# Kernel optimization log

Hardware: AMD Instinct MI355X
Metric: run time of the kernel (lower is better)

The kernel has to match this reference:

```python
import jax, jax.numpy as jnp
import numpy as np

B, T, D, H, E = 2, 1024, 1024, 4096, 8


def setup_inputs() -> dict:
    key = jax.random.key(0)
    ks = jax.random.split(key, 6)
    x = jax.random.normal(ks[0], (B, T, D), dtype=jnp.float32)
    padding_mask = jnp.zeros((B, T), dtype=bool)
    # Gate: Linear(D, E, bias=False) -> weight (E, D)
    Wg = jax.random.normal(ks[1], (E, D), dtype=jnp.float32) * (1.0 / np.sqrt(D))
    # Stacked expert FFN params (torch Linear layout: weight (out, in))
    W1 = jax.random.normal(ks[2], (E, H, D), dtype=jnp.float32) * (1.0 / np.sqrt(D))
    b1 = jax.random.normal(ks[3], (E, H), dtype=jnp.float32) * 0.01
    W2 = jax.random.normal(ks[4], (E, D, H), dtype=jnp.float32) * (1.0 / np.sqrt(H))
    b2 = jax.random.normal(ks[5], (E, D), dtype=jnp.float32) * 0.01
    return {"x": x, "padding_mask": padding_mask, "Wg": Wg, "W1": W1, "b1": b1, "W2": W2, "b2": b2}


def _top2_gate(xt, pm, Wg):
    # xt: (nt, D) flattened tokens, pm: (nt,) bool padding mask
    nt, ec = xt.shape[0], Wg.shape[0]
    logits = (xt @ Wg.T).astype(jnp.float32)            # use_fp32=True
    gate_value = jax.nn.softmax(logits, axis=-1)        # (nt, E)
    gate_value = jnp.where(pm[:, None], 0.0, gate_value)
    top2_idx = jax.lax.top_k(gate_value, 2)[1]          # (nt, 2)
    keep = jax.nn.one_hot(top2_idx, ec, dtype=bool).any(axis=1)  # (nt, E) True at top1/top2
    gate_weights = jnp.where(keep, gate_value, 0.0)
    s = gate_weights.sum(axis=1, keepdims=True)
    s = jnp.where(s == 0.0, 1.0, s)
    gate_weights = gate_weights / s
    # load-balance loss: fraction of top-1 assignments vs mean gate prob per expert
    nt_real = (~pm).sum().astype(jnp.float32)
    top1_counts = (jax.nn.one_hot(top2_idx[:, 0], ec, dtype=jnp.float32)
                   * (~pm)[:, None].astype(jnp.float32)).sum(axis=0)  # (E,)
    lb_loss = ec * ((top1_counts / nt_real) * (gate_value.sum(axis=0) / nt_real)).sum()
    return lb_loss, gate_weights, gate_value


def reference(x, padding_mask, Wg, W1, b1, W2, b2):
    Bx, Tx, Dx = x.shape
    xt = x.reshape(-1, Dx)                   # (nt, D)
    pm = padding_mask.reshape(-1)            # (nt,)
    lb_loss, gw, gate_value = _top2_gate(xt, pm, Wg)
    gw = gw.astype(x.dtype)                  # (nt, E)
    # Expert FFNs (dense over experts; routing weights are zero except top-2)
    h = jax.nn.relu(jnp.einsum('nd,ehd->neh', xt, W1) + b1)   # (nt, E, H)
    y = jnp.einsum('neh,edh->ned', h, W2) + b2                # (nt, E, D)
    out = jnp.einsum('ne,ned->nd', gw, y).reshape(Bx, Tx, Dx)
    return out, gate_value, lb_loss
```

## Files before the change

kernel.cpp:

```cpp
#include <hip/hip_runtime.h>
#include <hip/hip_bf16.h>
#include <stdint.h>


#define NTOK 2048
#define DDIM 1024
#define HDIM 4096
#define NEXP 8
#define KSPLIT 2
#define CONVB 1024
#define GATEB (NTOK / 4)
#define ZEROB 512

typedef float  f32x4  __attribute__((ext_vector_type(4)));
typedef __bf16 bf16x8 __attribute__((ext_vector_type(8)));
typedef __bf16 bf16x4 __attribute__((ext_vector_type(4)));

typedef const __attribute__((address_space(1))) void g1_t;
typedef __attribute__((address_space(3))) void l3_t;
__device__ __forceinline__ void gld16(const void* g, void* l) {
  __builtin_amdgcn_global_load_lds((g1_t*)g, (l3_t*)l, 16, 0, 0);
}

__device__ __forceinline__ void conv_body(int bid, const float* __restrict__ src,
                                          __bf16* __restrict__ dst, long n8) {
  long i = (long)bid * 256 + threadIdx.x;
  long stride = (long)CONVB * 256;
  for (; i < n8; i += stride) {
    f32x4 a = ((const f32x4*)src)[2 * i];
    f32x4 b = ((const f32x4*)src)[2 * i + 1];
    bf16x8 o;
#pragma unroll
    for (int q = 0; q < 4; ++q) { o[q] = (__bf16)a[q]; o[q + 4] = (__bf16)b[q]; }
    ((bf16x8*)dst)[i] = o;
  }
}

__device__ __forceinline__ void zero_body(int bid, float* __restrict__ y, long n4) {
  long i = (long)bid * 256 + threadIdx.x;
  long stride = (long)ZEROB * 256;
  for (; i < n4; i += stride) ((f32x4*)y)[i] = (f32x4){0.f, 0.f, 0.f, 0.f};
}

__device__ __forceinline__ void gate_body(int bid, const float* __restrict__ x,
                                          const unsigned char* __restrict__ pmask,
                                          const float* __restrict__ Wg,
                                          float* __restrict__ gate_out,
                                          int* __restrict__ tix, float* __restrict__ twt,
                                          __bf16* __restrict__ xbf) {
  int wave = threadIdx.x >> 6, lane = threadIdx.x & 63;
  int t = bid * 4 + wave;
  const f32x4* x4 = (const f32x4*)(x + (size_t)t * DDIM);
  const f32x4* w4 = (const f32x4*)Wg;
  bf16x4* xb4 = (bf16x4*)(xbf + (size_t)t * DDIM);
  float acc[NEXP];
#pragma unroll
  for (int e = 0; e < NEXP; ++e) acc[e] = 0.f;
#pragma unroll
  for (int i = 0; i < 4; ++i) {
    f32x4 xv = x4[i * 64 + lane];
    bf16x4 xo;
#pragma unroll
    for (int q = 0; q < 4; ++q) xo[q] = (__bf16)xv[q];
    xb4[i * 64 + lane] = xo;
#pragma unroll
    for (int e = 0; e < NEXP; ++e) {
      f32x4 wv = w4[e * 256 + i * 64 + lane];
      acc[e] += xv[0]*wv[0] + xv[1]*wv[1] + xv[2]*wv[2] + xv[3]*wv[3];
    }
  }
#pragma unroll
  for (int e = 0; e < NEXP; ++e) {
    float v = acc[e];
#pragma unroll
    for (int off = 32; off > 0; off >>= 1) v += __shfl_xor(v, off, 64);
    acc[e] = v;
  }
  if (lane == 0) {
    bool pm = pmask[t] != 0;
    float m = acc[0];
#pragma unroll
    for (int e = 1; e < NEXP; ++e) m = fmaxf(m, acc[e]);
    float g[NEXP]; float s = 0.f;
#pragma unroll
    for (int e = 0; e < NEXP; ++e) { g[e] = expf(acc[e] - m); s += g[e]; }
    float inv = 1.f / s;
#pragma unroll
    for (int e = 0; e < NEXP; ++e) g[e] *= inv;
    if (pm) {
#pragma unroll
      for (int e = 0; e < NEXP; ++e) g[e] = 0.f;
    }
    int i1 = 0;
#pragma unroll
    for (int e = 1; e < NEXP; ++e) if (g[e] > g[i1]) i1 = e;
    int i2 = -1;
#pragma unroll
    for (int e = 0; e < NEXP; ++e) if (e != i1 && (i2 < 0 || g[e] > g[i2])) i2 = e;
    float w1 = g[i1], w2 = g[i2], ss = w1 + w2;
    if (ss == 0.f) ss = 1.f;
    w1 /= ss; w2 /= ss;
#pragma unroll
    for (int e = 0; e < NEXP; ++e) gate_out[(size_t)t * NEXP + e] = g[e];
    tix[2*t] = i1; tix[2*t+1] = i2;
    twt[2*t] = w1; twt[2*t+1] = w2;
  }
}

__global__ __launch_bounds__(256)
void preA_kernel(const float* __restrict__ x, const unsigned char* __restrict__ pmask,
                 const float* __restrict__ Wg, float* __restrict__ gate_out,
                 int* __restrict__ tix, float* __restrict__ twt,
                 __bf16* __restrict__ xbf, const float* __restrict__ W1,
                 __bf16* __restrict__ w1bf, float* __restrict__ out)
{
  int bid = blockIdx.x;
  if (bid < CONVB) { conv_body(bid, W1, w1bf, (long)NEXP * HDIM * DDIM / 8); return; }
  bid -= CONVB;
  if (bid < GATEB) { gate_body(bid, x, pmask, Wg, gate_out, tix, twt, xbf); return; }
  bid -= GATEB;
  zero_body(bid, out, (long)NTOK * DDIM / 4);
}

__global__ __launch_bounds__(256)
void conv_kernel(const float* __restrict__ src, __bf16* __restrict__ dst, long n8)
{
  conv_body(blockIdx.x, src, dst, n8);
}

__global__ __launch_bounds__(1024)
void stats_kernel(const float* __restrict__ gate_out, const int* __restrict__ tix,
                  const unsigned char* __restrict__ pmask,
                  int* __restrict__ ecount, int* __restrict__ offs,
                  int* __restrict__ fill, float* __restrict__ lb_out)
{
  int tid = threadIdx.x, lane = tid & 63, wv = tid >> 6;
  float lg[NEXP]; float lt1[NEXP]; int lec[NEXP]; float ln = 0.f;
#pragma unroll
  for (int e = 0; e < NEXP; ++e) { lg[e] = 0.f; lt1[e] = 0.f; lec[e] = 0; }
#pragma unroll
  for (int it = 0; it < NTOK / 1024; ++it) {
    int t = tid + it * 1024;
    f32x4 g0 = ((const f32x4*)(gate_out + (size_t)t * NEXP))[0];
    f32x4 g1 = ((const f32x4*)(gate_out + (size_t)t * NEXP))[1];
    lg[0] += g0[0]; lg[1] += g0[1]; lg[2] += g0[2]; lg[3] += g0[3];
    lg[4] += g1[0]; lg[5] += g1[1]; lg[6] += g1[2]; lg[7] += g1[3];
    if (!pmask[t]) {
      int i1 = tix[2*t], i2 = tix[2*t+1];
      lt1[i1] += 1.f; lec[i1] += 1; lec[i2] += 1; ln += 1.f;
    }
  }
#pragma unroll
  for (int e = 0; e < NEXP; ++e) {
#pragma unroll
    for (int off = 32; off > 0; off >>= 1) {
      lg[e]  += __shfl_xor(lg[e],  off, 64);
      lt1[e] += __shfl_xor(lt1[e], off, 64);
      lec[e] += __shfl_xor(lec[e], off, 64);
    }
  }
#pragma unroll
  for (int off = 32; off > 0; off >>= 1) ln += __shfl_xor(ln, off, 64);
  __shared__ float sg[16][NEXP], st[16][NEXP], sn[16];
  __shared__ int   se[16][NEXP];
  if (lane == 0) {
#pragma unroll
    for (int e = 0; e < NEXP; ++e) { sg[wv][e] = lg[e]; st[wv][e] = lt1[e]; se[wv][e] = lec[e]; }
    sn[wv] = ln;
  }
  __syncthreads();
  if (tid == 0) {
    float G[NEXP] = {0}, T1[NEXP] = {0}; int EC[NEXP] = {0}; float N = 0.f;
    for (int w = 0; w < 16; ++w) {
      N += sn[w];
#pragma unroll
      for (int e = 0; e < NEXP; ++e) { G[e] += sg[w][e]; T1[e] += st[w][e]; EC[e] += se[w][e]; }
    }
    int o = 0;
    for (int e = 0; e < NEXP; ++e) { ecount[e] = EC[e]; offs[e] = o; o += EC[e]; fill[e] = 0; }
    if (N <= 0.f) N = 1.f;
    float lb = 0.f;
    for (int e = 0; e < NEXP; ++e) lb += (T1[e] / N) * (G[e] / N);
    lb_out[0] = (float)NEXP * lb;
  }
}

__global__ __launch_bounds__(256)
void compact_kernel(const unsigned char* __restrict__ pmask, const int* __restrict__ tix,
                    const float* __restrict__ twt, const int* __restrict__ offs,
                    int* __restrict__ fill, int* __restrict__ tok_list,
                    float* __restrict__ wgt_list)
{
  int t = blockIdx.x * 256 + threadIdx.x;
  int lane = threadIdx.x & 63;
  bool pm = pmask[t] != 0;
#pragma unroll
  for (int j = 0; j < 2; ++j) {
    int e = pm ? -1 : tix[2*t + j];
    int pos = -1;
#pragma unroll
    for (int ex = 0; ex < NEXP; ++ex) {
      unsigned long long mask = __ballot(e == ex);
      if (mask) {
        int leader = (int)(__ffsll((long long)mask) - 1);
        int base = 0;
        if (lane == leader) base = atomicAdd(&fill[ex], (int)__popcll(mask));
        base = __shfl(base, leader, 64);
        if (e == ex)
          pos = offs[ex] + base + (int)__popcll(mask & ((1ull << lane) - 1ull));
      }
    }
    if (e >= 0) { tok_list[pos] = t; wgt_list[pos] = twt[2*t + j]; }
  }
}


__global__ __launch_bounds__(256)
void gemm1_kernel(const __bf16* __restrict__ xbf, const __bf16* __restrict__ w1bf,
                  const float* __restrict__ b1, const int* __restrict__ ecount,
                  const int* __restrict__ offs, const int* __restrict__ tok_list,
                  __bf16* __restrict__ hbuf)
{
  const int NTILE = HDIM / 128;
  const int MTILE = NTOK / 128;
  int bid = blockIdx.x;
  int e = bid / (MTILE * NTILE);
  int rem = bid % (MTILE * NTILE);
  int mt = rem / NTILE, nt = rem % NTILE;
  int cnt = ecount[e];
  if (mt * 128 >= cnt) return;
  int off = offs[e];

  __shared__ __bf16 As[3][128 * 32];
  __shared__ __bf16 Bs[3][128 * 32];

  int tid = threadIdx.x, lane = tid & 63, wave = tid >> 6;
  int wm = wave >> 1, wn = wave & 1;

  const __bf16* aP[2];
  const __bf16* bP[2];
#pragma unroll
  for (int c = 0; c < 2; ++c) {
    int row = c * 64 + (tid >> 2);
    int cd = (tid & 3) ^ ((row >> 1) & 3);
    int mrow = mt * 128 + row;
    int tok = tok_list[off + ((mrow < cnt) ? mrow : 0)];
    aP[c] = xbf + (size_t)tok * DDIM + cd * 8;
    bP[c] = w1bf + (size_t)e * HDIM * DDIM + (size_t)(nt * 128 + row) * DDIM + cd * 8;
  }
  int cg = ((lane >> 4) ^ ((lane >> 1) & 3)) << 3;

  f32x4 acc[4][4];
#pragma unroll
  for (int m = 0; m < 4; ++m)
#pragma unroll
    for (int n = 0; n < 4; ++n) acc[m][n] = (f32x4){0.f, 0.f, 0.f, 0.f};

  const int NIT = DDIM / 32;
#pragma unroll
  for (int pt = 0; pt < 2; ++pt)
#pragma unroll
    for (int c = 0; c < 2; ++c) {
      gld16(aP[c] + pt * 32, &As[pt][(c * 64 + wave * 16) * 32]);
      gld16(bP[c] + pt * 32, &Bs[pt][(c * 64 + wave * 16) * 32]);
    }

  for (int it = 0; it < NIT; ++it) {
    int cur = it % 3;
    if (it + 1 < NIT) asm volatile("s_waitcnt vmcnt(4)" ::: "memory");
    else              asm volatile("s_waitcnt vmcnt(0)" ::: "memory");
    __builtin_amdgcn_s_barrier();
    __builtin_amdgcn_sched_barrier(0);
    if (it + 2 < NIT) {
      int nb = (it + 2) % 3;
      int k0 = (it + 2) * 32;
#pragma unroll
      for (int c = 0; c < 2; ++c) {
        gld16(aP[c] + k0, &As[nb][(c * 64 + wave * 16) * 32]);
        gld16(bP[c] + k0, &Bs[nb][(c * 64 + wave * 16) * 32]);
      }
    }
    bf16x8 af[4], bfr[4];
#pragma unroll
    for (int m = 0; m < 4; ++m) af[m]  = *(const bf16x8*)&As[cur][(wm*64 + m*16 + (lane & 15)) * 32 + cg];
#pragma unroll
    for (int n = 0; n < 4; ++n) bfr[n] = *(const bf16x8*)&Bs[cur][(wn*64 + n*16 + (lane & 15)) * 32 + cg];
#pragma unroll
    for (int m = 0; m < 4; ++m)
#pragma unroll
      for (int n = 0; n < 4; ++n)
        acc[m][n] = __builtin_amdgcn_mfma_f32_16x16x32_bf16(af[m], bfr[n], acc[m][n], 0, 0, 0);
  }

#pragma unroll
  for (int n = 0; n < 4; ++n) {
    int col = nt * 128 + wn * 64 + n * 16 + (lane & 15);
    float bias = b1[e * HDIM + col];
#pragma unroll
    for (int m = 0; m < 4; ++m) {
#pragma unroll
      for (int j = 0; j < 4; ++j) {
        int mr = mt * 128 + wm * 64 + m * 16 + ((lane >> 4) << 2) + j;
        if (mr < cnt) {
          float v = fmaxf(acc[m][n][j] + bias, 0.f);
          hbuf[(size_t)(off + mr) * HDIM + col] = (__bf16)v;
        }
      }
    }
  }
}

__global__ __launch_bounds__(256)
void gemm2_kernel(const __bf16* __restrict__ hbuf, const __bf16* __restrict__ w2bf,
                  const float* __restrict__ b2, const int* __restrict__ ecount,
                  const int* __restrict__ offs, const int* __restrict__ tok_list,
                  const float* __restrict__ wgt_list, float* __restrict__ out)
{
  const int NTILE = DDIM / 128;
  const int MTILE = NTOK / 128;
  int bid = blockIdx.x;
  int e = bid / (MTILE * NTILE * KSPLIT);
  int rem = bid % (MTILE * NTILE * KSPLIT);
  int mt = rem / (NTILE * KSPLIT);
  int rem2 = rem % (NTILE * KSPLIT);
  int nt = rem2 / KSPLIT, kc = rem2 % KSPLIT;
  int cnt = ecount[e];
  if (mt * 128 >= cnt) return;
  int off = offs[e];

  __shared__ __bf16 As[3][128 * 32];
  __shared__ __bf16 Bs[3][128 * 32];

  int tid = threadIdx.x, lane = tid & 63, wave = tid >> 6;
  int wm = wave >> 1, wn = wave & 1;

  const __bf16* aP[2];
  const __bf16* bP[2];
#pragma unroll
  for (int c = 0; c < 2; ++c) {
    int row = c * 64 + (tid >> 2);
    int cd = (tid & 3) ^ ((row >> 1) & 3);
    aP[c] = hbuf + (size_t)(off + mt * 128 + row) * HDIM + cd * 8;
    bP[c] = w2bf + (size_t)e * DDIM * HDIM + (size_t)(nt * 128 + row) * HDIM + cd * 8;
  }
  int cg = ((lane >> 4) ^ ((lane >> 1) & 3)) << 3;

  f32x4 acc[4][4];
#pragma unroll
  for (int m = 0; m < 4; ++m)
#pragma unroll
    for (int n = 0; n < 4; ++n) acc[m][n] = (f32x4){0.f, 0.f, 0.f, 0.f};

  const int KCH = HDIM / KSPLIT;
  const int NIT = KCH / 32;
  int kbeg = kc * KCH;
#pragma unroll
  for (int pt = 0; pt < 2; ++pt)
#pragma unroll
    for (int c = 0; c < 2; ++c) {
      gld16(aP[c] + kbeg + pt * 32, &As[pt][(c * 64 + wave * 16) * 32]);
      gld16(bP[c] + kbeg + pt * 32, &Bs[pt][(c * 64 + wave * 16) * 32]);
    }

  for (int it = 0; it < NIT; ++it) {
    int cur = it % 3;
    if (it + 1 < NIT) asm volatile("s_waitcnt vmcnt(4)" ::: "memory");
    else              asm volatile("s_waitcnt vmcnt(0)" ::: "memory");
    __builtin_amdgcn_s_barrier();
    __builtin_amdgcn_sched_barrier(0);
    if (it + 2 < NIT) {
      int nb = (it + 2) % 3;
      int k0 = kbeg + (it + 2) * 32;
#pragma unroll
      for (int c = 0; c < 2; ++c) {
        gld16(aP[c] + k0, &As[nb][(c * 64 + wave * 16) * 32]);
        gld16(bP[c] + k0, &Bs[nb][(c * 64 + wave * 16) * 32]);
      }
    }
    bf16x8 af[4], bfr[4];
#pragma unroll
    for (int m = 0; m < 4; ++m) af[m]  = *(const bf16x8*)&As[cur][(wm*64 + m*16 + (lane & 15)) * 32 + cg];
#pragma unroll
    for (int n = 0; n < 4; ++n) bfr[n] = *(const bf16x8*)&Bs[cur][(wn*64 + n*16 + (lane & 15)) * 32 + cg];
#pragma unroll
    for (int m = 0; m < 4; ++m)
#pragma unroll
      for (int n = 0; n < 4; ++n)
        acc[m][n] = __builtin_amdgcn_mfma_f32_16x16x32_bf16(af[m], bfr[n], acc[m][n], 0, 0, 0);
  }

  float b2v[4];
#pragma unroll
  for (int n = 0; n < 4; ++n) {
    int col = nt * 128 + wn * 64 + n * 16 + (lane & 15);
    b2v[n] = (kc == 0) ? b2[e * DDIM + col] : 0.f;
  }
#pragma unroll
  for (int m = 0; m < 4; ++m) {
#pragma unroll
    for (int j = 0; j < 4; ++j) {
      int mr = mt * 128 + wm * 64 + m * 16 + ((lane >> 4) << 2) + j;
      if (mr >= cnt) continue;
      int slot = off + mr;
      int tok = tok_list[slot];
      float w = wgt_list[slot];
      float* obase = out + (size_t)tok * DDIM;
#pragma unroll
      for (int n = 0; n < 4; ++n) {
        int col = nt * 128 + wn * 64 + n * 16 + (lane & 15);
        atomicAdd(obase + col, w * (acc[m][n][j] + b2v[n]));
      }
    }
  }
}

extern "C" void kernel_launch(void* const* d_in, const int* in_sizes, int n_in,
                              void* d_out, int out_size, void* d_ws, size_t ws_size,
                              hipStream_t stream)
{
  const float* x  = (const float*)d_in[0];
  const unsigned char* pm = (const unsigned char*)d_in[1];
  const float* Wg = (const float*)d_in[2];
  const float* W1 = (const float*)d_in[3];
  const float* b1 = (const float*)d_in[4];
  const float* W2 = (const float*)d_in[5];
  const float* b2 = (const float*)d_in[6];
  float* out = (float*)d_out;
  float* gate_out = out + (size_t)NTOK * DDIM;
  float* lb_out = gate_out + (size_t)NTOK * NEXP;

  char* w = (char*)d_ws;
  int*   ecount   = (int*)(w + 0);
  int*   offs     = (int*)(w + 64);
  int*   fill     = (int*)(w + 128);
  int*   tix      = (int*)(w + 512);
  float* twt      = (float*)(w + 512 + 16384);
  int*   tok_list = (int*)(w + 512 + 32768);
  float* wgt_list = (float*)(w + 512 + 49152);
  uintptr_t p = ((uintptr_t)(w + 512 + 65536) + 255) & ~(uintptr_t)255;
  __bf16* xbf  = (__bf16*)p;
  p += (size_t)NTOK * DDIM * 2;
  __bf16* w1bf = (__bf16*)p;
  p += (size_t)NEXP * HDIM * DDIM * 2;
  __bf16* hbuf = (__bf16*)p;
  p += (size_t)(2 * NTOK + 128) * HDIM * 2;
  __bf16* w2bf_sep = (__bf16*)p;
  size_t need = (size_t)((char*)(w2bf_sep + (size_t)NEXP * DDIM * HDIM) - w);
  __bf16* w2bf = (ws_size >= need) ? w2bf_sep : w1bf;

  preA_kernel<<<CONVB + GATEB + ZEROB, 256, 0, stream>>>(x, pm, Wg, gate_out, tix, twt, xbf, W1, w1bf, out);
  stats_kernel<<<1, 1024, 0, stream>>>(gate_out, tix, pm, ecount, offs, fill, lb_out);
  compact_kernel<<<NTOK / 256, 256, 0, stream>>>(pm, tix, twt, offs, fill, tok_list, wgt_list);
  gemm1_kernel<<<NEXP * (NTOK / 128) * (HDIM / 128), 256, 0, stream>>>(
      xbf, w1bf, b1, ecount, offs, tok_list, hbuf);
  conv_kernel<<<CONVB, 256, 0, stream>>>(W2, w2bf, (long)NEXP * DDIM * HDIM / 8);
  gemm2_kernel<<<NEXP * (NTOK / 128) * (DDIM / 128) * KSPLIT, 256, 0, stream>>>(
      hbuf, w2bf, b2, ecount, offs, tok_list, wgt_list, out);
}
```

Measured before the change: 249.5 us.

## Fuse W2 conversion into prologue, merge compaction into stats, raise KSPLIT

When the workspace is large enough, the W2 fp32-to-bf16 conversion now runs as extra blocks in the prologue kernel instead of as a separate launch after gemm1. The token compaction pass moves into the single-block stats kernel and uses shared-memory fill counters, which removes a launch and the global atomics. The gemm2 K-split is raised from 2 to 4 for more parallelism, at the cost of more atomic output accumulation. Compaction now runs in one block, which serialises that work.

New measurement: 277.9 us. 1.11x slower.

```diff
diff --git a/kernel.cpp b/kernel.cpp
--- a/kernel.cpp
+++ b/kernel.cpp
@@ -7,7 +7,7 @@
 #define DDIM 1024
 #define HDIM 4096
 #define NEXP 8
-#define KSPLIT 2
+#define KSPLIT 4
 #define CONVB 1024
 #define GATEB (NTOK / 4)
 #define ZEROB 512
@@ -112,10 +112,16 @@
                  const float* __restrict__ Wg, float* __restrict__ gate_out,
                  int* __restrict__ tix, float* __restrict__ twt,
                  __bf16* __restrict__ xbf, const float* __restrict__ W1,
-                 __bf16* __restrict__ w1bf, float* __restrict__ out)
+                 __bf16* __restrict__ w1bf, const float* __restrict__ W2,
+                 __bf16* __restrict__ w2bf, float* __restrict__ out)
 {
   int bid = blockIdx.x;
   if (bid < CONVB) { conv_body(bid, W1, w1bf, (long)NEXP * HDIM * DDIM / 8); return; }
+  bid -= CONVB;
+  if (bid < CONVB) {
+    if (W2) conv_body(bid, W2, w2bf, (long)NEXP * DDIM * HDIM / 8);
+    return;
+  }
   bid -= CONVB;
   if (bid < GATEB) { gate_body(bid, x, pmask, Wg, gate_out, tix, twt, xbf); return; }
   bid -= GATEB;
@@ -130,9 +136,10 @@
 
 __global__ __launch_bounds__(1024)
 void stats_kernel(const float* __restrict__ gate_out, const int* __restrict__ tix,
-                  const unsigned char* __restrict__ pmask,
-                  int* __restrict__ ecount, int* __restrict__ offs,
-                  int* __restrict__ fill, float* __restrict__ lb_out)
+                  const float* __restrict__ twt, const unsigned char* __restrict__ pmask,
+                  int* __restrict__ ecount, int* __restrict__ offs_g,
+                  float* __restrict__ lb_out, int* __restrict__ tok_list,
+                  float* __restrict__ wgt_list)
 {
   int tid = threadIdx.x, lane = tid & 63, wv = tid >> 6;
   float lg[NEXP]; float lt1[NEXP]; int lec[NEXP]; float ln = 0.f;
@@ -163,6 +170,7 @@
   for (int off = 32; off > 0; off >>= 1) ln += __shfl_xor(ln, off, 64);
   __shared__ float sg[16][NEXP], st[16][NEXP], sn[16];
   __shared__ int   se[16][NEXP];
+  __shared__ int   soffs[NEXP], sfill[NEXP];
   if (lane == 0) {
 #pragma unroll
     for (int e = 0; e < NEXP; ++e) { sg[wv][e] = lg[e]; st[wv][e] = lt1[e]; se[wv][e] = lec[e]; }
@@ -177,40 +185,38 @@
       for (int e = 0; e < NEXP; ++e) { G[e] += sg[w][e]; T1[e] += st[w][e]; EC[e] += se[w][e]; }
     }
     int o = 0;
-    for (int e = 0; e < NEXP; ++e) { ecount[e] = EC[e]; offs[e] = o; o += EC[e]; fill[e] = 0; }
+    for (int e = 0; e < NEXP; ++e) {
+      ecount[e] = EC[e]; offs_g[e] = o; soffs[e] = o; sfill[e] = 0; o += EC[e];
+    }
     if (N <= 0.f) N = 1.f;
     float lb = 0.f;
     for (int e = 0; e < NEXP; ++e) lb += (T1[e] / N) * (G[e] / N);
     lb_out[0] = (float)NEXP * lb;
   }
-}
-
-__global__ __launch_bounds__(256)
-void compact_kernel(const unsigned char* __restrict__ pmask, const int* __restrict__ tix,
-                    const float* __restrict__ twt, const int* __restrict__ offs,
-                    int* __restrict__ fill, int* __restrict__ tok_list,
-                    float* __restrict__ wgt_list)
-{
-  int t = blockIdx.x * 256 + threadIdx.x;
-  int lane = threadIdx.x & 63;
-  bool pm = pmask[t] != 0;
-#pragma unroll
-  for (int j = 0; j < 2; ++j) {
-    int e = pm ? -1 : tix[2*t + j];
-    int pos = -1;
-#pragma unroll
-    for (int ex = 0; ex < NEXP; ++ex) {
-      unsigned long long mask = __ballot(e == ex);
-      if (mask) {
-        int leader = (int)(__ffsll((long long)mask) - 1);
-        int base = 0;
-        if (lane == leader) base = atomicAdd(&fill[ex], (int)__popcll(mask));
-        base = __shfl(base, leader, 64);
-        if (e == ex)
-          pos = offs[ex] + base + (int)__popcll(mask & ((1ull << lane) - 1ull));
+  __syncthreads();
+#pragma unroll
+  for (int it = 0; it < NTOK / 1024; ++it) {
+    int t = tid + it * 1024;
+    bool pm = pmask[t] != 0;
+#pragma unroll
+    for (int j = 0; j < 2; ++j) {
+      int e = pm ? -1 : tix[2*t + j];
+#pragma unroll
+      for (int ex = 0; ex < NEXP; ++ex) {
+        unsigned long long mask = __ballot(e == ex);
+        if (mask) {
+          int leader = (int)(__ffsll((long long)mask) - 1);
+          int base = 0;
+          if (lane == leader) base = atomicAdd(&sfill[ex], (int)__popcll(mask));
+          base = __shfl(base, leader, 64);
+          if (e == ex) {
+            int pos = soffs[ex] + base + (int)__popcll(mask & ((1ull << lane) - 1ull));
+            tok_list[pos] = t;
+            wgt_list[pos] = twt[2*t + j];
+          }
+        }
       }
     }
-    if (e >= 0) { tok_list[pos] = t; wgt_list[pos] = twt[2*t + j]; }
   }
 }
 
@@ -432,7 +438,6 @@
   char* w = (char*)d_ws;
   int*   ecount   = (int*)(w + 0);
   int*   offs     = (int*)(w + 64);
-  int*   fill     = (int*)(w + 128);
   int*   tix      = (int*)(w + 512);
   float* twt      = (float*)(w + 512 + 16384);
   int*   tok_list = (int*)(w + 512 + 32768);
@@ -446,14 +451,17 @@
   p += (size_t)(2 * NTOK + 128) * HDIM * 2;
   __bf16* w2bf_sep = (__bf16*)p;
   size_t need = (size_t)((char*)(w2bf_sep + (size_t)NEXP * DDIM * HDIM) - w);
-  __bf16* w2bf = (ws_size >= need) ? w2bf_sep : w1bf;
-
-  preA_kernel<<<CONVB + GATEB + ZEROB, 256, 0, stream>>>(x, pm, Wg, gate_out, tix, twt, xbf, W1, w1bf, out);
-  stats_kernel<<<1, 1024, 0, stream>>>(gate_out, tix, pm, ecount, offs, fill, lb_out);
-  compact_kernel<<<NTOK / 256, 256, 0, stream>>>(pm, tix, twt, offs, fill, tok_list, wgt_list);
+  bool sep = (ws_size >= need);
+  __bf16* w2bf = sep ? w2bf_sep : w1bf;
+
+  preA_kernel<<<2 * CONVB + GATEB + ZEROB, 256, 0, stream>>>(
+      x, pm, Wg, gate_out, tix, twt, xbf, W1, w1bf,
+      sep ? W2 : (const float*)nullptr, w2bf, out);
+  stats_kernel<<<1, 1024, 0, stream>>>(gate_out, tix, twt, pm, ecount, offs, lb_out,
+                                       tok_list, wgt_list);
   gemm1_kernel<<<NEXP * (NTOK / 128) * (HDIM / 128), 256, 0, stream>>>(
       xbf, w1bf, b1, ecount, offs, tok_list, hbuf);
-  conv_kernel<<<CONVB, 256, 0, stream>>>(W2, w2bf, (long)NEXP * DDIM * HDIM / 8);
+  if (!sep) conv_kernel<<<CONVB, 256, 0, stream>>>(W2, w2bf, (long)NEXP * DDIM * HDIM / 8);
   gemm2_kernel<<<NEXP * (NTOK / 128) * (DDIM / 128) * KSPLIT, 256, 0, stream>>>(
       hbuf, w2bf, b2, ecount, offs, tok_list, wgt_list, out);
 }
```
